# Performance work log

Measured on AMD Instinct MI355X. Metric: run time of the kernel, lower is better.

## Reference

```python
import jax, jax.numpy as jnp
import numpy as np

# spk_param = (thr, temp, damp); dt, tau from module config
THR, TEMP, DAMP = 0.4, 0.1, 0.9
DT, TAU = 0.1, 1.0


@jax.custom_vjp
def spike(v, u):
    # Stochastic Bernoulli spike: sigmoid(temp*v) > uniform noise
    return (jax.nn.sigmoid(TEMP * v) > u).astype(v.dtype)

def _spike_fwd(v, u):
    return spike(v, u), v

def _spike_bwd(v, g):
    # Faithful to the torch Spike.backward: returns the pseudo-derivative
    # damp*clamp(1-|v|,0) directly (the original ignores grad_output).
    return (DAMP * jnp.maximum(1.0 - jnp.abs(v), 0.0), jnp.zeros_like(v))

spike.defvjp(_spike_fwd, _spike_bwd)


def setup_inputs() -> dict:
    key = jax.random.key(0)
    k1, k2, k3, k4, k5 = jax.random.split(key, 5)
    B_, T, IN, N, OUT = 128, 512, 128, 512, 128
    inputs = jax.random.normal(k1, (B_, T, IN), dtype=jnp.float32)
    rand_u = jax.random.uniform(k2, (B_, T, N), dtype=jnp.float32)
    init_std = 1.0
    J = jax.random.normal(k3, (N, N), dtype=jnp.float32) * (init_std / np.sqrt(N))
    Bw = jax.random.normal(k4, (N, IN), dtype=jnp.float32)  # input projection (non-trainable in torch)
    W = jax.random.normal(k5, (OUT, N), dtype=jnp.float32) * (1.0 / np.sqrt(N))
    return {"inputs": inputs, "rand_u": rand_u, "J": J, "Bw": Bw, "W": W}


def reference(inputs, rand_u, J, Bw, W):
    B_, T, _ = inputs.shape
    N = J.shape[0]
    alpha = DT / TAU
    decay = 1.0 - alpha

    def step(carry, xs):
        v, z = carry
        x_t, u_t = xs  # [B, IN], [B, N]
        v_new = decay * v + alpha * z
        lamb = jnp.tanh(v_new) @ J.T + x_t @ Bw.T  # [B, N]
        z_new = spike((lamb - THR) / THR, u_t)
        out = lamb @ W.T  # [B, OUT]
        return (v_new, z_new), (v_new, z_new, out)

    v0 = jnp.zeros((B_, N), dtype=inputs.dtype)
    z0 = jnp.zeros((B_, N), dtype=inputs.dtype)
    xs = (jnp.swapaxes(inputs, 0, 1), jnp.swapaxes(rand_u, 0, 1))  # time-major
    _, (vs, zs, outs) = jax.lax.scan(step, (v0, z0), xs)

    vt = jnp.concatenate([v0[:, None, :], jnp.swapaxes(vs, 0, 1)], axis=1)  # [B, T+1, N]
    zt = jnp.concatenate([z0[:, None, :], jnp.swapaxes(zs, 0, 1)], axis=1)  # [B, T+1, N]
    output_seq = jnp.swapaxes(outs, 0, 1)  # [B, T, OUT]
    return vt, zt, output_seq
```

## Files before the change

kernel.cpp:

```cpp
#include <hip/hip_runtime.h>


typedef __attribute__((ext_vector_type(8))) short short8x;
typedef __attribute__((ext_vector_type(4))) float f32x4;
typedef __attribute__((ext_vector_type(4))) int i32x4;

#define OFF_JQK  (0u)
#define OFF_BWH  (262144u)
#define OFF_BWL  (393216u)
#define OFF_G    (524288u)
#define OFF_M    (786432u)
#define OFF_GPK  (851968u)
#define OFF_MPK  (983040u)

#define SC_J 640.0f
#define SC_S 166.0f

__device__ __forceinline__ unsigned short f2bf(float f) {
  union { float f; unsigned u; } a; a.f = f;
  unsigned r = a.u + 0x7FFFu + ((a.u >> 16) & 1u);
  return (unsigned short)(r >> 16);
}
__device__ __forceinline__ float bf2f(unsigned short h) {
  union { unsigned u; float f; } a; a.u = ((unsigned)h) << 16;
  return a.f;
}
__device__ __forceinline__ float thr_of(float u) {
  return __builtin_fmaf(4.0f, __logf(u / (1.0f - u)), 0.4f);
}
__device__ __forceinline__ float fast_tanh_pos(float x) {
  const float e2 = __expf(x + x);
  return 1.0f - 2.0f / (e2 + 1.0f);
}

__launch_bounds__(512)
__global__ void jwm_kernel(const float* __restrict__ J, const float* __restrict__ Bw,
                           const float* __restrict__ W, unsigned char* __restrict__ ws) {
  __shared__ float wrow[512];
  const int o = blockIdx.x;
  const int tid = threadIdx.x;
  wrow[tid] = W[(size_t)o * 512 + tid];
  __syncthreads();
  const int k = tid;
  const int i = tid & 127;
  float g = 0.0f, m = 0.0f;
  for (int n = 0; n < 512; ++n) {
    const float wv = wrow[n];
    g = __builtin_fmaf(wv, J[(size_t)n * 512 + k], g);
    m = __builtin_fmaf(wv, Bw[(size_t)n * 128 + i], m);
  }
  ((float*)(ws + OFF_G))[(size_t)o * 512 + k] = g;
  if (tid < 128) ((float*)(ws + OFF_M))[(size_t)o * 128 + i] = m;
}

__global__ void pack_kernel(const float* __restrict__ J, const float* __restrict__ Bw,
                            unsigned char* __restrict__ ws) {
  const int id = blockIdx.x * 256 + threadIdx.x;
  if (id < 16384) {
    const int idx = id;
    const int n = idx & 511, kg = idx >> 9, k0 = kg * 16;
    unsigned dw[4];
#pragma unroll
    for (int d = 0; d < 4; ++d) {
      unsigned x = 0;
#pragma unroll
      for (int p = 0; p < 4; ++p) {
        const float jv = J[(size_t)n * 512 + k0 + 4 * d + p];
        int q = __float2int_rn(jv * SC_J);
        q = q > 127 ? 127 : (q < -127 ? -127 : q);
        x |= ((unsigned)(q & 255)) << (8 * p);
      }
      dw[d] = x;
    }
    uint4 out; out.x = dw[0]; out.y = dw[1]; out.z = dw[2]; out.w = dw[3];
    ((uint4*)(ws + OFF_JQK))[idx] = out;
  } else if (id < 24576) {
    const int idx = id - 16384;
    const int n = idx & 511, kg = idx >> 9, k0 = kg * 8;
    unsigned short* bwh = (unsigned short*)(ws + OFF_BWH);
    unsigned short* bwl = (unsigned short*)(ws + OFF_BWL);
    for (int e = 0; e < 8; ++e) {
      const float x = Bw[(size_t)n * 128 + k0 + e];
      const unsigned short h = f2bf(x);
      bwh[(size_t)idx * 8 + e] = h;
      bwl[(size_t)idx * 8 + e] = f2bf(x - bf2f(h));
    }
  } else if (id < 32768) {
    const int idx = id - 24576;
    const int o = idx & 127, kg = idx >> 7, k0 = kg * 8;
    const float* G = (const float*)(ws + OFF_G);
    unsigned short* gpk = (unsigned short*)(ws + OFF_GPK);
    for (int e = 0; e < 8; ++e) gpk[(size_t)idx * 8 + e] = f2bf(G[(size_t)o * 512 + k0 + e]);
  } else {
    const int idx = id - 32768;
    const int o = idx & 127, kg = idx >> 7, k0 = kg * 8;
    const float* M = (const float*)(ws + OFF_M);
    unsigned short* mpk = (unsigned short*)(ws + OFF_MPK);
    for (int e = 0; e < 8; ++e) mpk[(size_t)idx * 8 + e] = f2bf(M[(size_t)o * 128 + k0 + e]);
  }
}

__launch_bounds__(256)
__global__ void xpd_kernel(const float* __restrict__ X, const float* __restrict__ U,
                           const unsigned char* __restrict__ ws, float* __restrict__ Dbuf) {
  __shared__ short Ah[64 * 136];
  __shared__ short Al[64 * 136];
  const unsigned short* bwh = (const unsigned short*)(ws + OFF_BWH);
  const unsigned short* bwl = (const unsigned short*)(ws + OFF_BWL);
  const int m0 = blockIdx.x * 64;
  const int n0 = blockIdx.y * 64;
  const int tid = threadIdx.x;
  for (int i = tid; i < 64 * 32; i += 256) {
    const int r = i >> 5, kq = i & 31;
    const float4 x4 = *(const float4*)(X + (size_t)(m0 + r) * 128 + kq * 4);
    short4 h4, l4; unsigned short h;
    h = f2bf(x4.x); h4.x = (short)h; l4.x = (short)f2bf(x4.x - bf2f(h));
    h = f2bf(x4.y); h4.y = (short)h; l4.y = (short)f2bf(x4.y - bf2f(h));
    h = f2bf(x4.z); h4.z = (short)h; l4.z = (short)f2bf(x4.z - bf2f(h));
    h = f2bf(x4.w); h4.w = (short)h; l4.w = (short)f2bf(x4.w - bf2f(h));
    *(short4*)(&Ah[r * 136 + kq * 4]) = h4;
    *(short4*)(&Al[r * 136 + kq * 4]) = l4;
  }
  __syncthreads();
  const int w = tid >> 6, l = tid & 63, lhi = l >> 4, llo = l & 15;
  const int rowA = 16 * w + llo;
  f32x4 a0 = {0,0,0,0}, a1 = {0,0,0,0}, a2 = {0,0,0,0}, a3 = {0,0,0,0};
#pragma unroll
  for (int kt = 0; kt < 4; ++kt) {
    const short8x ah = *(const short8x*)(&Ah[rowA * 136 + kt * 32 + lhi * 8]);
    const short8x al = *(const short8x*)(&Al[rowA * 136 + kt * 32 + lhi * 8]);
#define XT(TI, ACC) { \
    const size_t bi = ((size_t)((kt * 4 + lhi) * 512 + n0 + TI * 16 + llo)) * 8; \
    const short8x bh = *(const short8x*)(bwh + bi); \
    const short8x bl = *(const short8x*)(bwl + bi); \
    ACC = __builtin_amdgcn_mfma_f32_16x16x32_bf16(ah, bh, ACC, 0, 0, 0); \
    ACC = __builtin_amdgcn_mfma_f32_16x16x32_bf16(al, bh, ACC, 0, 0, 0); \
    ACC = __builtin_amdgcn_mfma_f32_16x16x32_bf16(ah, bl, ACC, 0, 0, 0); }
    XT(0, a0) XT(1, a1) XT(2, a2) XT(3, a3)
#undef XT
  }
  const int n = n0 + llo;
#pragma unroll
  for (int r = 0; r < 4; ++r) {
    const int bt = m0 + 16 * w + lhi * 4 + r;
    const float* urow = U + (size_t)bt * 512;
    float* drow = Dbuf + (size_t)bt * 512;
    drow[n]      = thr_of(urow[n])      - a0[r];
    drow[n + 16] = thr_of(urow[n + 16]) - a1[r];
    drow[n + 32] = thr_of(urow[n + 32]) - a2[r];
    drow[n + 48] = thr_of(urow[n + 48]) - a3[r];
  }
}

__launch_bounds__(512, 1)
__global__ void recur_kernel(const unsigned char* __restrict__ ws,
                             const float* __restrict__ Dbuf,
                             unsigned char* __restrict__ z8) {
  __shared__ unsigned char s_sm[2][512];
  __shared__ int lam_s[512];
  const int b = blockIdx.x;
  const int tid = threadIdx.x;
  const int w = tid >> 6, l = tid & 63;
  const int lhi = l >> 4, llo = l & 15;
  const int n = tid;

  i32x4 ji[4][8];
#pragma unroll
  for (int kt = 0; kt < 8; ++kt) {
    const unsigned base = (unsigned)(kt * 4 + lhi) * 512u + (unsigned)(w * 64 + llo);
#pragma unroll
    for (int j = 0; j < 4; ++j) {
      const unsigned char* p = ws + OFF_JQK + (size_t)(base + 16u * j) * 16u;
      asm volatile("global_load_dwordx4 %0, %1, off" : "=v"(ji[j][kt]) : "v"(p));
    }
  }
  asm volatile("s_waitcnt vmcnt(0)" ::: "memory");

  const float SC = 1.0f / (SC_J * SC_S);
  float v = 0.0f;
  unsigned zprev = 0u;
  const float* Dp = Dbuf + (size_t)b * 262144 + n;
  unsigned char* zwg = z8 + (size_t)b * 262144 + n;

  float dc[8], dnx[8];
#pragma unroll
  for (int i = 0; i < 8; ++i) dc[i] = Dp[(size_t)i * 512];

  for (int c = 0; c < 64; ++c) {
    const int t0 = c * 8;
#pragma unroll
    for (int i = 0; i < 8; ++i) dnx[i] = Dp[(size_t)(t0 + 8 + i) * 512];
#pragma unroll
    for (int i = 0; i < 8; ++i) {
      const int t = t0 + i;
      v = __builtin_fmaf(0.9f, v, zprev ? 0.1f : 0.0f);
      const float s = fast_tanh_pos(v);
      const unsigned q = (unsigned)__float2int_rn(s * SC_S);
      s_sm[t & 1][n] = (unsigned char)q;
      asm volatile("s_waitcnt lgkmcnt(0)\n\ts_barrier" ::: "memory");
      i32x4 a0 = {0,0,0,0}, a1 = {0,0,0,0}, a2 = {0,0,0,0}, a3 = {0,0,0,0};
#pragma unroll
      for (int kt = 0; kt < 8; ++kt) {
        const i32x4 bf = *(const i32x4*)(&s_sm[t & 1][kt * 64 + lhi * 16]);
        a0 = __builtin_amdgcn_mfma_i32_16x16x64_i8(ji[0][kt], bf, a0, 0, 0, 0);
        a1 = __builtin_amdgcn_mfma_i32_16x16x64_i8(ji[1][kt], bf, a1, 0, 0, 0);
        a2 = __builtin_amdgcn_mfma_i32_16x16x64_i8(ji[2][kt], bf, a2, 0, 0, 0);
        a3 = __builtin_amdgcn_mfma_i32_16x16x64_i8(ji[3][kt], bf, a3, 0, 0, 0);
      }
      if (llo == 0) {
        *(i32x4*)(lam_s + w * 64 +  0 + lhi * 4) = a0;
        *(i32x4*)(lam_s + w * 64 + 16 + lhi * 4) = a1;
        *(i32x4*)(lam_s + w * 64 + 32 + lhi * 4) = a2;
        *(i32x4*)(lam_s + w * 64 + 48 + lhi * 4) = a3;
      }
      asm volatile("s_waitcnt lgkmcnt(0)" ::: "memory");
      const float lam = (float)lam_s[n] * SC;
      const unsigned z = (lam > dc[i]) ? 1u : 0u;
      zwg[(size_t)t * 512] = (unsigned char)z;
      zprev = z;
    }
#pragma unroll
    for (int i = 0; i < 8; ++i) dc[i] = dnx[i];
  }
}

__launch_bounds__(512)
__global__ void vsz_kernel(const float* __restrict__ X, const unsigned char* __restrict__ ws,
                           float* __restrict__ vt, float* __restrict__ zt,
                           float* __restrict__ op) {
  __shared__ unsigned zl[8192];
  __shared__ unsigned short sl[64 * 520];
  __shared__ unsigned short xl[64 * 136];
  const int b = blockIdx.x;
  const int tid = threadIdx.x;
  const int w = tid >> 6, l = tid & 63, lhi = l >> 4, llo = l & 15;
  const unsigned short* gpk = (const unsigned short*)(ws + OFF_GPK);
  const unsigned short* mpk = (const unsigned short*)(ws + OFF_MPK);
  const unsigned char* z8 = (const unsigned char*)op;

  float v = 0.0f;
  unsigned zprev = 0u;
  vt[((size_t)b * 513) * 512 + tid] = 0.0f;
  zt[((size_t)b * 513) * 512 + tid] = 0.0f;

  for (int c = 0; c < 8; ++c) {
    const uint4* src = (const uint4*)(z8 + (size_t)b * 262144 + (size_t)c * 32768);
#pragma unroll
    for (int i = 0; i < 4; ++i) ((uint4*)zl)[i * 512 + tid] = src[i * 512 + tid];
#pragma unroll
    for (int i = 0; i < 4; ++i) {
      const int idx = i * 512 + tid;
      const int r = idx >> 5, c4 = (idx & 31) * 4;
      const float4 x4 = *(const float4*)(X + ((size_t)b * 512 + c * 64 + r) * 128 + c4);
      short4 h4;
      h4.x = (short)f2bf(x4.x); h4.y = (short)f2bf(x4.y);
      h4.z = (short)f2bf(x4.z); h4.w = (short)f2bf(x4.w);
      *(short4*)(xl + r * 136 + c4) = h4;
    }
    __syncthreads();
    const unsigned char* zb = (const unsigned char*)zl;
    float* vrow = vt + ((size_t)b * 513 + c * 64 + 1) * 512 + tid;
    float* zrow = zt + ((size_t)b * 513 + c * 64 + 1) * 512 + tid;
#pragma unroll 8
    for (int tl = 0; tl < 64; ++tl) {
      v = __builtin_fmaf(0.9f, v, zprev ? 0.1f : 0.0f);
      const unsigned z = zb[tl * 512 + tid];
      vrow[(size_t)tl * 512] = v;
      zrow[(size_t)tl * 512] = z ? 1.0f : 0.0f;
      sl[tl * 520 + tid] = f2bf(fast_tanh_pos(v));
      zprev = z;
    }
    __syncthreads();
    const int m = w >> 1, oh = (w & 1) * 4;
    f32x4 a0 = {0,0,0,0}, a1 = {0,0,0,0}, a2 = {0,0,0,0}, a3 = {0,0,0,0};
#pragma unroll
    for (int kt = 0; kt < 16; ++kt) {
      const short8x A = *(const short8x*)(sl + (m * 16 + llo) * 520 + kt * 32 + lhi * 8);
#define GT(TI, ACC) { \
      const short8x B = *(const short8x*)(gpk + ((size_t)((kt * 4 + lhi) * 128 + (oh + TI) * 16 + llo)) * 8); \
      ACC = __builtin_amdgcn_mfma_f32_16x16x32_bf16(A, B, ACC, 0, 0, 0); }
      GT(0, a0) GT(1, a1) GT(2, a2) GT(3, a3)
#undef GT
    }
#pragma unroll
    for (int kt = 0; kt < 4; ++kt) {
      const short8x A = *(const short8x*)(xl + (m * 16 + llo) * 136 + kt * 32 + lhi * 8);
#define MT(TI, ACC) { \
      const short8x B = *(const short8x*)(mpk + ((size_t)((kt * 4 + lhi) * 128 + (oh + TI) * 16 + llo)) * 8); \
      ACC = __builtin_amdgcn_mfma_f32_16x16x32_bf16(A, B, ACC, 0, 0, 0); }
      MT(0, a0) MT(1, a1) MT(2, a2) MT(3, a3)
#undef MT
    }
    float* obase = op + ((size_t)b * 512 + c * 64 + m * 16 + lhi * 4) * 128 + llo;
#pragma unroll
    for (int r = 0; r < 4; ++r) {
      float* orow = obase + (size_t)r * 128;
      orow[(oh + 0) * 16] = a0[r];
      orow[(oh + 1) * 16] = a1[r];
      orow[(oh + 2) * 16] = a2[r];
      orow[(oh + 3) * 16] = a3[r];
    }
    __syncthreads();
  }
}

extern "C" void kernel_launch(void* const* d_in, const int* in_sizes, int n_in,
                              void* d_out, int out_size, void* d_ws, size_t ws_size,
                              hipStream_t stream) {
  const float* X  = (const float*)d_in[0];
  const float* U  = (const float*)d_in[1];
  const float* J  = (const float*)d_in[2];
  const float* Bw = (const float*)d_in[3];
  const float* W  = (const float*)d_in[4];
  float* vt = (float*)d_out;
  float* zt = vt + (size_t)128 * 513 * 512;
  float* op = vt + (size_t)2 * 128 * 513 * 512;
  unsigned char* ws = (unsigned char*)d_ws;
  float* Dbuf = vt;
  unsigned char* z8 = (unsigned char*)op;

  jwm_kernel<<<128, 512, 0, stream>>>(J, Bw, W, ws);
  pack_kernel<<<136, 256, 0, stream>>>(J, Bw, ws);
  xpd_kernel<<<dim3(1024, 8), 256, 0, stream>>>(X, U, ws, Dbuf);
  recur_kernel<<<128, 512, 0, stream>>>(ws, Dbuf, z8);
  vsz_kernel<<<128, 512, 0, stream>>>(X, ws, vt, zt, op);
}
```

Baseline: 806.9 us.

## Replace recurrent int8 MFMA matvec with per-thread dot4 and speculative tanh

```diff
diff --git a/kernel.cpp b/kernel.cpp
--- a/kernel.cpp
+++ b/kernel.cpp
@@ -31,6 +31,15 @@
 __device__ __forceinline__ float fast_tanh_pos(float x) {
   const float e2 = __expf(x + x);
   return 1.0f - 2.0f / (e2 + 1.0f);
+}
+__device__ __forceinline__ int sdot4(unsigned a, unsigned b, int acc) {
+#if __has_builtin(__builtin_amdgcn_sdot4)
+  return __builtin_amdgcn_sdot4((int)a, (int)b, acc, false);
+#else
+  int r;
+  asm("v_dot4_i32_i8 %0, %1, %2, %3" : "=v"(r) : "v"(a), "v"(b), "v"(acc));
+  return r;
+#endif
 }
 
 __launch_bounds__(512)
@@ -156,35 +165,30 @@
 __global__ void recur_kernel(const unsigned char* __restrict__ ws,
                              const float* __restrict__ Dbuf,
                              unsigned char* __restrict__ z8) {
-  __shared__ unsigned char s_sm[2][512];
-  __shared__ int lam_s[512];
+  __shared__ __align__(16) unsigned char s_sm[2][512];
   const int b = blockIdx.x;
   const int tid = threadIdx.x;
-  const int w = tid >> 6, l = tid & 63;
-  const int lhi = l >> 4, llo = l & 15;
-  const int n = tid;
-
-  i32x4 ji[4][8];
-#pragma unroll
-  for (int kt = 0; kt < 8; ++kt) {
-    const unsigned base = (unsigned)(kt * 4 + lhi) * 512u + (unsigned)(w * 64 + llo);
-#pragma unroll
-    for (int j = 0; j < 4; ++j) {
-      const unsigned char* p = ws + OFF_JQK + (size_t)(base + 16u * j) * 16u;
-      asm volatile("global_load_dwordx4 %0, %1, off" : "=v"(ji[j][kt]) : "v"(p));
-    }
+
+  uint4 jr[32];
+#pragma unroll
+  for (int kg = 0; kg < 32; ++kg) {
+    const unsigned char* p = ws + OFF_JQK + ((size_t)kg * 512 + (size_t)tid) * 16;
+    asm volatile("global_load_dwordx4 %0, %1, off" : "=v"(jr[kg]) : "v"(p));
   }
   asm volatile("s_waitcnt vmcnt(0)" ::: "memory");
 
   const float SC = 1.0f / (SC_J * SC_S);
-  float v = 0.0f;
+  const float* Dp = Dbuf + (size_t)b * 262144 + tid;
+  unsigned char* zwg = z8 + (size_t)b * 262144 + tid;
+
+  float dc[8], dnx[8];
+#pragma unroll
+  for (int i = 0; i < 8; ++i) dc[i] = Dp[(size_t)i * 512];
+
   unsigned zprev = 0u;
-  const float* Dp = Dbuf + (size_t)b * 262144 + n;
-  unsigned char* zwg = z8 + (size_t)b * 262144 + n;
-
-  float dc[8], dnx[8];
-#pragma unroll
-  for (int i = 0; i < 8; ++i) dc[i] = Dp[(size_t)i * 512];
+  float v0 = 0.0f, v1 = 0.1f;
+  unsigned q0 = (unsigned)__float2int_rn(fast_tanh_pos(v0) * SC_S);
+  unsigned q1 = (unsigned)__float2int_rn(fast_tanh_pos(v1) * SC_S);
 
   for (int c = 0; c < 64; ++c) {
     const int t0 = c * 8;
@@ -193,28 +197,24 @@
 #pragma unroll
     for (int i = 0; i < 8; ++i) {
       const int t = t0 + i;
-      v = __builtin_fmaf(0.9f, v, zprev ? 0.1f : 0.0f);
-      const float s = fast_tanh_pos(v);
-      const unsigned q = (unsigned)__float2int_rn(s * SC_S);
-      s_sm[t & 1][n] = (unsigned char)q;
+      const unsigned q = zprev ? q1 : q0;
+      const float v = zprev ? v1 : v0;
+      s_sm[t & 1][tid] = (unsigned char)q;
       asm volatile("s_waitcnt lgkmcnt(0)\n\ts_barrier" ::: "memory");
-      i32x4 a0 = {0,0,0,0}, a1 = {0,0,0,0}, a2 = {0,0,0,0}, a3 = {0,0,0,0};
-#pragma unroll
-      for (int kt = 0; kt < 8; ++kt) {
-        const i32x4 bf = *(const i32x4*)(&s_sm[t & 1][kt * 64 + lhi * 16]);
-        a0 = __builtin_amdgcn_mfma_i32_16x16x64_i8(ji[0][kt], bf, a0, 0, 0, 0);
-        a1 = __builtin_amdgcn_mfma_i32_16x16x64_i8(ji[1][kt], bf, a1, 0, 0, 0);
-        a2 = __builtin_amdgcn_mfma_i32_16x16x64_i8(ji[2][kt], bf, a2, 0, 0, 0);
-        a3 = __builtin_amdgcn_mfma_i32_16x16x64_i8(ji[3][kt], bf, a3, 0, 0, 0);
+      v0 = 0.9f * v; v1 = v0 + 0.1f;
+      q0 = (unsigned)__float2int_rn(fast_tanh_pos(v0) * SC_S);
+      q1 = (unsigned)__float2int_rn(fast_tanh_pos(v1) * SC_S);
+      const uint4* sp = (const uint4*)s_sm[t & 1];
+      int a0 = 0, a1 = 0, a2 = 0, a3 = 0;
+#pragma unroll
+      for (int g = 0; g < 32; ++g) {
+        const uint4 sv = sp[g];
+        a0 = sdot4(jr[g].x, sv.x, a0);
+        a1 = sdot4(jr[g].y, sv.y, a1);
+        a2 = sdot4(jr[g].z, sv.z, a2);
+        a3 = sdot4(jr[g].w, sv.w, a3);
       }
-      if (llo == 0) {
-        *(i32x4*)(lam_s + w * 64 +  0 + lhi * 4) = a0;
-        *(i32x4*)(lam_s + w * 64 + 16 + lhi * 4) = a1;
-        *(i32x4*)(lam_s + w * 64 + 32 + lhi * 4) = a2;
-        *(i32x4*)(lam_s + w * 64 + 48 + lhi * 4) = a3;
-      }
-      asm volatile("s_waitcnt lgkmcnt(0)" ::: "memory");
-      const float lam = (float)lam_s[n] * SC;
+      const float lam = (float)((a0 + a1) + (a2 + a3)) * SC;
       const unsigned z = (lam > dc[i]) ? 1u : 0u;
       zwg[(size_t)t * 512] = (unsigned char)z;
       zprev = z;
```

After: 824.3 us. +2.2%, slower.
